# Performance work log

Hardware: AMD Instinct MI355X
Metric: run time of the kernel (lower is better)

Reference implementation:

```python
import jax, jax.numpy as jnp
import numpy as np

N_NODES = 100000
N_EDGES = 800000

def setup_inputs() -> dict:
    key = jax.random.key(0)
    ks = jax.random.split(key, 8)
    x = jax.random.normal(ks[0], (N_NODES, 500), dtype=jnp.float32)
    edge_index = jax.random.randint(ks[1], (2, N_EDGES), 0, N_NODES, dtype=jnp.int64)
    s = lambda k, shape, fan_in: jax.random.normal(k, shape, jnp.float32) / np.sqrt(fan_in)
    return {
        "x": x,
        "edge_index": edge_index,
        "W1_l": s(ks[2], (500, 20), 500),
        "W1_r": s(ks[3], (500, 20), 500),
        "b1": jnp.zeros((20,), jnp.float32),
        "W2_l": s(ks[4], (20, 3), 20),
        "W2_r": s(ks[5], (20, 3), 20),
        "b2": jnp.zeros((3,), jnp.float32),
    }

def _sage_conv(x, src, dst, W_l, W_r, b, deg_inv):
    # mean-aggregate neighbor features (x_j = x[src]) at dst, PyG default 'mean'
    agg = jax.ops.segment_sum(x[src], dst, num_segments=x.shape[0])  # [N, F]
    agg = agg * deg_inv[:, None]
    return agg @ W_l + b + x @ W_r

def reference(x, edge_index, W1_l, W1_r, b1, W2_l, W2_r, b2):
    src, dst = edge_index[0], edge_index[1]
    deg = jax.ops.segment_sum(jnp.ones_like(dst, dtype=x.dtype), dst, num_segments=x.shape[0])
    deg_inv = 1.0 / jnp.maximum(deg, 1.0)
    h = _sage_conv(x, src, dst, W1_l, W1_r, b1, deg_inv)
    h = jax.nn.relu(h)
    # F.dropout(p=0.5, training=self.training): identity in eval mode
    out = _sage_conv(h, src, dst, W2_l, W2_r, b2, deg_inv)
    return out
```

## Files before the change

kernel.cpp:

```cpp
#include <hip/hip_runtime.h>

#define F_IN  500
#define F_HID 20
#define F_OUT 3
#define KT    16
#define NT    3

typedef __attribute__((ext_vector_type(8))) short short8;
typedef __attribute__((ext_vector_type(4))) float v4f;

__device__ __forceinline__ unsigned f2bf(float f) {
    unsigned u = __float_as_uint(f);
    u = u + 0x7fffu + ((u >> 16) & 1u);
    return u >> 16;
}
__device__ __forceinline__ float bf2f(unsigned h) {
    return __uint_as_float(h << 16);
}

__global__ void k_degree(const int* __restrict__ dst, int* __restrict__ deg, int E) {
    int i = blockIdx.x * blockDim.x + threadIdx.x;
    if (i < E) atomicAdd(&deg[dst[i]], 1);
}

__global__ void k_scan_blk(const int* __restrict__ deg, int* __restrict__ rowstart,
                           int* __restrict__ blocksums, int N) {
    __shared__ int lds[256];
    int tid = threadIdx.x;
    int base = blockIdx.x * 1024 + tid * 4;
    int4 v = make_int4(0, 0, 0, 0);
    if (base + 3 < N) {
        v = *(const int4*)(deg + base);
    } else {
        if (base + 0 < N) v.x = deg[base + 0];
        if (base + 1 < N) v.y = deg[base + 1];
        if (base + 2 < N) v.z = deg[base + 2];
        if (base + 3 < N) v.w = deg[base + 3];
    }
    int tsum = v.x + v.y + v.z + v.w;
    lds[tid] = tsum;
    __syncthreads();
    for (int off = 1; off < 256; off <<= 1) {
        int t = (tid >= off) ? lds[tid - off] : 0;
        __syncthreads();
        lds[tid] += t;
        __syncthreads();
    }
    int excl = lds[tid] - tsum;
    if (tid == 255) blocksums[blockIdx.x] = lds[255];
    int r = excl;
    if (base + 0 < N) rowstart[base + 0] = r; r += v.x;
    if (base + 1 < N) rowstart[base + 1] = r; r += v.y;
    if (base + 2 < N) rowstart[base + 2] = r; r += v.z;
    if (base + 3 < N) rowstart[base + 3] = r;
}

__global__ void k_scan_sums(int* __restrict__ blocksums, int NB) {
    __shared__ int lds[256];
    int tid = threadIdx.x;
    int v = (tid < NB) ? blocksums[tid] : 0;
    lds[tid] = v;
    __syncthreads();
    for (int off = 1; off < 256; off <<= 1) {
        int t = (tid >= off) ? lds[tid - off] : 0;
        __syncthreads();
        lds[tid] += t;
        __syncthreads();
    }
    if (tid < NB) blocksums[tid] = lds[tid] - v;
}

__global__ void k_scan_add(int* __restrict__ rowstart, const int* __restrict__ blocksums, int N) {
    int i = blockIdx.x * blockDim.x + threadIdx.x;
    if (i < N) rowstart[i] += blocksums[i >> 10];
}

__global__ void k_fill(const int* __restrict__ src, const int* __restrict__ dst,
                       int* __restrict__ rowstart, int* __restrict__ csr, int E) {
    int e = blockIdx.x * blockDim.x + threadIdx.x;
    if (e >= E) return;
    int pos = atomicAdd(&rowstart[dst[e]], 1);
    csr[pos] = src[e];
}

__global__ void k_prepB(const float* __restrict__ Wl, const float* __restrict__ Wr,
                        unsigned short* __restrict__ Bhi, unsigned short* __restrict__ Blo) {
    int i = blockIdx.x * blockDim.x + threadIdx.x;
    if (i >= KT * NT * 64) return;
    int lane = i & 63;
    int ntk  = i >> 6;
    int nt   = ntk % NT;
    int kt   = ntk / NT;
    int n     = nt * 16 + (lane & 15);
    int kbase = kt * 32 + (lane >> 4) * 8;
#pragma unroll
    for (int j = 0; j < 8; ++j) {
        int k = kbase + j;
        float w = 0.f;
        if (k < F_IN && n < 2 * F_HID)
            w = (n < F_HID) ? Wl[k * F_HID + n] : Wr[k * F_HID + (n - F_HID)];
        unsigned h = f2bf(w);
        Bhi[(size_t)i * 8 + j] = (unsigned short)h;
        Blo[(size_t)i * 8 + j] = (unsigned short)f2bf(w - bf2f(h));
    }
}

__global__ __launch_bounds__(256) void k_gemm1(const float* __restrict__ x,
        const unsigned short* __restrict__ Bhi, const unsigned short* __restrict__ Blo,
        float* __restrict__ y, int N) {
    __shared__ unsigned short xhi[64 * 32];
    __shared__ unsigned short xlo[64 * 32];
    const int tid  = threadIdx.x;
    const int lane = tid & 63;
    const int wv   = tid >> 6;
    const int row0 = blockIdx.x * 64;

    v4f acc[NT];
#pragma unroll
    for (int nt = 0; nt < NT; ++nt) { acc[nt][0]=0.f; acc[nt][1]=0.f; acc[nt][2]=0.f; acc[nt][3]=0.f; }

    const int srow = tid >> 3;
    const int skc  = (tid & 7) * 4;
    const int arow = wv * 16 + (lane & 15);
    const int ak   = (lane >> 4) * 8;

    for (int kt = 0; kt < KT; ++kt) {
#pragma unroll
        for (int hh = 0; hh < 2; ++hh) {
            int rl   = srow + hh * 32;
            int grow = row0 + rl;
            int gk   = kt * 32 + skc;
            float4 v = make_float4(0.f, 0.f, 0.f, 0.f);
            if (grow < N && gk + 3 < F_IN)
                v = *(const float4*)(x + (size_t)grow * F_IN + gk);
            unsigned h0 = f2bf(v.x), h1 = f2bf(v.y), h2 = f2bf(v.z), h3 = f2bf(v.w);
            unsigned l0 = f2bf(v.x - bf2f(h0));
            unsigned l1 = f2bf(v.y - bf2f(h1));
            unsigned l2 = f2bf(v.z - bf2f(h2));
            unsigned l3 = f2bf(v.w - bf2f(h3));
            *(uint2*)&xhi[rl * 32 + skc] = make_uint2(h0 | (h1 << 16), h2 | (h3 << 16));
            *(uint2*)&xlo[rl * 32 + skc] = make_uint2(l0 | (l1 << 16), l2 | (l3 << 16));
        }
        __syncthreads();
        short8 Ah = *(const short8*)&xhi[arow * 32 + ak];
        short8 Al = *(const short8*)&xlo[arow * 32 + ak];
#pragma unroll
        for (int nt = 0; nt < NT; ++nt) {
            size_t fo = (((size_t)kt * NT + nt) * 64 + lane) * 8;
            short8 Bh = *(const short8*)(Bhi + fo);
            short8 Bl = *(const short8*)(Blo + fo);
            acc[nt] = __builtin_amdgcn_mfma_f32_16x16x32_bf16(Ah, Bh, acc[nt], 0, 0, 0);
            acc[nt] = __builtin_amdgcn_mfma_f32_16x16x32_bf16(Ah, Bl, acc[nt], 0, 0, 0);
            acc[nt] = __builtin_amdgcn_mfma_f32_16x16x32_bf16(Al, Bh, acc[nt], 0, 0, 0);
        }
        __syncthreads();
    }
    int rloc = wv * 16 + (lane >> 4) * 4;
#pragma unroll
    for (int nt = 0; nt < NT; ++nt) {
        int col = nt * 16 + (lane & 15);
        if (col < 2 * F_HID) {
#pragma unroll
            for (int rg = 0; rg < 4; ++rg) {
                int grow = row0 + rloc + rg;
                if (grow < N) y[(size_t)grow * 40 + col] = acc[nt][rg];
            }
        }
    }
}

__global__ void k_agg1(const int* __restrict__ rowend, const int* __restrict__ deg,
                       const int* __restrict__ csr, const float* __restrict__ y,
                       float* __restrict__ agg1, int N) {
    int i = blockIdx.x * blockDim.x + threadIdx.x;
    if (i >= N * 5) return;
    int n = i / 5;
    int cg = i - n * 5;
    int d = deg[n];
    int beg = rowend[n] - d;
    float4 acc = make_float4(0.f, 0.f, 0.f, 0.f);
    for (int j = 0; j < d; ++j) {
        int s = csr[beg + j];
        float4 v = *(const float4*)(y + (size_t)s * 40 + cg * 4);
        acc.x += v.x; acc.y += v.y; acc.z += v.z; acc.w += v.w;
    }
    *(float4*)(agg1 + (size_t)n * F_HID + cg * 4) = acc;
}

__global__ void k_layer1(const int* __restrict__ deg,
                         const float* __restrict__ agg1,
                         const float* __restrict__ y,
                         const float* __restrict__ b1,
                         const float* __restrict__ W2l,
                         const float* __restrict__ W2r,
                         float* __restrict__ zl, float* __restrict__ zr, int N) {
    int n = blockIdx.x * blockDim.x + threadIdx.x;
    if (n >= N) return;
    float di = 1.0f / fmaxf((float)deg[n], 1.0f);
    float h[F_HID];
    const float4* pa = (const float4*)(agg1 + (size_t)n * F_HID);
    const float4* pr = (const float4*)(y + (size_t)n * 40 + F_HID);
#pragma unroll
    for (int q = 0; q < F_HID / 4; ++q) {
        float4 a = pa[q];
        float4 r = pr[q];
        h[4*q+0] = fmaxf(a.x * di + b1[4*q+0] + r.x, 0.f);
        h[4*q+1] = fmaxf(a.y * di + b1[4*q+1] + r.y, 0.f);
        h[4*q+2] = fmaxf(a.z * di + b1[4*q+2] + r.z, 0.f);
        h[4*q+3] = fmaxf(a.w * di + b1[4*q+3] + r.w, 0.f);
    }
    float zlo[F_OUT] = {0.f, 0.f, 0.f};
    float zro[F_OUT] = {0.f, 0.f, 0.f};
#pragma unroll
    for (int c = 0; c < F_HID; ++c) {
#pragma unroll
        for (int o = 0; o < F_OUT; ++o) {
            zlo[o] += h[c] * W2l[c * F_OUT + o];
            zro[o] += h[c] * W2r[c * F_OUT + o];
        }
    }
#pragma unroll
    for (int o = 0; o < F_OUT; ++o) {
        zl[(size_t)n * F_OUT + o] = zlo[o];
        zr[(size_t)n * F_OUT + o] = zro[o];
    }
}

__global__ void k_agg2_final(const int* __restrict__ rowend, const int* __restrict__ deg,
                             const int* __restrict__ csr, const float* __restrict__ zl,
                             const float* __restrict__ zr, const float* __restrict__ b2,
                             float* __restrict__ out, int N) {
    int n = blockIdx.x * blockDim.x + threadIdx.x;
    if (n >= N) return;
    int d = deg[n];
    int beg = rowend[n] - d;
    float a0 = 0.f, a1 = 0.f, a2 = 0.f;
    for (int j = 0; j < d; ++j) {
        int s = csr[beg + j];
        const float* z = zl + (size_t)s * F_OUT;
        a0 += z[0]; a1 += z[1]; a2 += z[2];
    }
    float di = 1.0f / fmaxf((float)d, 1.0f);
    out[(size_t)n * F_OUT + 0] = a0 * di + b2[0] + zr[(size_t)n * F_OUT + 0];
    out[(size_t)n * F_OUT + 1] = a1 * di + b2[1] + zr[(size_t)n * F_OUT + 1];
    out[(size_t)n * F_OUT + 2] = a2 * di + b2[2] + zr[(size_t)n * F_OUT + 2];
}

extern "C" void kernel_launch(void* const* d_in, const int* in_sizes, int n_in,
                              void* d_out, int out_size, void* d_ws, size_t ws_size,
                              hipStream_t stream) {
    const float* x   = (const float*)d_in[0];
    const int*   ei  = (const int*)d_in[1];
    const float* W1l = (const float*)d_in[2];
    const float* W1r = (const float*)d_in[3];
    const float* b1  = (const float*)d_in[4];
    const float* W2l = (const float*)d_in[5];
    const float* W2r = (const float*)d_in[6];
    const float* b2  = (const float*)d_in[7];
    float* out = (float*)d_out;

    const int N = in_sizes[0] / F_IN;
    const int E = in_sizes[1] / 2;
    const int* src = ei;
    const int* dst = ei + E;

    int*   wsi      = (int*)d_ws;
    int*   deg      = wsi;
    int*   rowstart = deg + N;
    int*   blocksums= rowstart + N;
    int*   csr      = blocksums + 256;
    float* y        = (float*)(csr + E);
    float* agg1     = y + (size_t)N * 40;
    float* zl       = agg1 + (size_t)N * F_HID;
    float* zr       = zl + (size_t)N * F_OUT;
    unsigned short* Bhi = (unsigned short*)(zr + (size_t)N * F_OUT);
    unsigned short* Blo = Bhi + (size_t)KT * NT * 64 * 8;

    hipMemsetAsync(deg, 0, (size_t)N * sizeof(int), stream);

    const int B = 256;
    const int NB = (N + 1023) / 1024;
    k_prepB     <<<(KT * NT * 64 + B - 1) / B, B, 0, stream>>>(W1l, W1r, Bhi, Blo);
    k_degree    <<<(E + B - 1) / B, B, 0, stream>>>(dst, deg, E);
    k_scan_blk  <<<NB, 256, 0, stream>>>(deg, rowstart, blocksums, N);
    k_scan_sums <<<1, 256, 0, stream>>>(blocksums, NB);
    k_scan_add  <<<(N + B - 1) / B, B, 0, stream>>>(rowstart, blocksums, N);
    k_fill      <<<(E + B - 1) / B, B, 0, stream>>>(src, dst, rowstart, csr, E);
    k_gemm1     <<<(N + 63) / 64, 256, 0, stream>>>(x, Bhi, Blo, y, N);
    k_agg1      <<<(N * 5 + B - 1) / B, B, 0, stream>>>(rowstart, deg, csr, y, agg1, N);
    k_layer1    <<<(N + B - 1) / B, B, 0, stream>>>(deg, agg1, y, b1, W2l, W2r, zl, zr, N);
    k_agg2_final<<<(N + B - 1) / B, B, 0, stream>>>(rowstart, deg, csr, zl, zr, b2, out, N);
}
```

Baseline: 436.4 us.

## Restructure GNN pipeline: fused prep, LDS-free GEMM, fused aggregation and layer1

```diff
diff --git a/kernel.cpp b/kernel.cpp
--- a/kernel.cpp
+++ b/kernel.cpp
@@ -18,12 +18,57 @@
     return __uint_as_float(h << 16);
 }
 
-__global__ void k_degree(const int* __restrict__ dst, int* __restrict__ deg, int E) {
-    int i = blockIdx.x * blockDim.x + threadIdx.x;
-    if (i < E) atomicAdd(&deg[dst[i]], 1);
-}
-
-__global__ void k_scan_blk(const int* __restrict__ deg, int* __restrict__ rowstart,
+__device__ __forceinline__ void cvt8(const float4 p, const float4 q, short8& hi, short8& lo) {
+    float vf[8] = {p.x, p.y, p.z, p.w, q.x, q.y, q.z, q.w};
+    union { unsigned u[4]; short8 s; } H, L;
+#pragma unroll
+    for (int t = 0; t < 4; ++t) {
+        unsigned u0 = __float_as_uint(vf[2*t]);
+        unsigned u1 = __float_as_uint(vf[2*t+1]);
+        unsigned r0 = u0 + 0x7fffu + ((u0 >> 16) & 1u);
+        unsigned r1 = u1 + 0x7fffu + ((u1 >> 16) & 1u);
+        float f0 = __uint_as_float(r0 & 0xffff0000u);
+        float f1 = __uint_as_float(r1 & 0xffff0000u);
+        float d0 = vf[2*t]   - f0;
+        float d1 = vf[2*t+1] - f1;
+        unsigned s0 = __float_as_uint(d0); s0 = s0 + 0x7fffu + ((s0 >> 16) & 1u);
+        unsigned s1 = __float_as_uint(d1); s1 = s1 + 0x7fffu + ((s1 >> 16) & 1u);
+        H.u[t] = (r0 >> 16) | (r1 & 0xffff0000u);
+        L.u[t] = (s0 >> 16) | (s1 & 0xffff0000u);
+    }
+    hi = H.s; lo = L.s;
+}
+
+__global__ void k_prep(const float* __restrict__ W1l, const float* __restrict__ W1r,
+                       unsigned short* __restrict__ Bhi, unsigned short* __restrict__ Blo,
+                       const int* __restrict__ dst, int* __restrict__ deg, int E) {
+    int b = blockIdx.x;
+    int tid = threadIdx.x;
+    if (b < (KT * NT * 64) / 256) {
+        int i = b * 256 + tid;
+        int lane = i & 63;
+        int ntk  = i >> 6;
+        int nt   = ntk % NT;
+        int kt   = ntk / NT;
+        int n     = nt * 16 + (lane & 15);
+        int kbase = kt * 32 + (lane >> 4) * 8;
+#pragma unroll
+        for (int j = 0; j < 8; ++j) {
+            int k = kbase + j;
+            float w = 0.f;
+            if (k < F_IN && n < 2 * F_HID)
+                w = (n < F_HID) ? W1l[k * F_HID + n] : W1r[k * F_HID + (n - F_HID)];
+            unsigned h = f2bf(w);
+            Bhi[(size_t)i * 8 + j] = (unsigned short)h;
+            Blo[(size_t)i * 8 + j] = (unsigned short)f2bf(w - bf2f(h));
+        }
+    } else {
+        int e = (b - (KT * NT * 64) / 256) * 256 + tid;
+        if (e < E) atomicAdd(&deg[dst[e]], 1);
+    }
+}
+
+__global__ void k_scan_blk(const int* __restrict__ deg, int* __restrict__ rowloc,
                            int* __restrict__ blocksums, int N) {
     __shared__ int lds[256];
     int tid = threadIdx.x;
@@ -49,10 +94,10 @@
     int excl = lds[tid] - tsum;
     if (tid == 255) blocksums[blockIdx.x] = lds[255];
     int r = excl;
-    if (base + 0 < N) rowstart[base + 0] = r; r += v.x;
-    if (base + 1 < N) rowstart[base + 1] = r; r += v.y;
-    if (base + 2 < N) rowstart[base + 2] = r; r += v.z;
-    if (base + 3 < N) rowstart[base + 3] = r;
+    if (base + 0 < N) rowloc[base + 0] = r; r += v.x;
+    if (base + 1 < N) rowloc[base + 1] = r; r += v.y;
+    if (base + 2 < N) rowloc[base + 2] = r; r += v.z;
+    if (base + 3 < N) rowloc[base + 3] = r;
 }
 
 __global__ void k_scan_sums(int* __restrict__ blocksums, int NB) {
@@ -70,180 +115,158 @@
     if (tid < NB) blocksums[tid] = lds[tid] - v;
 }
 
-__global__ void k_scan_add(int* __restrict__ rowstart, const int* __restrict__ blocksums, int N) {
-    int i = blockIdx.x * blockDim.x + threadIdx.x;
-    if (i < N) rowstart[i] += blocksums[i >> 10];
-}
-
 __global__ void k_fill(const int* __restrict__ src, const int* __restrict__ dst,
-                       int* __restrict__ rowstart, int* __restrict__ csr, int E) {
+                       int* __restrict__ rowloc, const int* __restrict__ bs,
+                       int* __restrict__ csr, int E) {
     int e = blockIdx.x * blockDim.x + threadIdx.x;
     if (e >= E) return;
-    int pos = atomicAdd(&rowstart[dst[e]], 1);
+    int dn = dst[e];
+    int pos = atomicAdd(&rowloc[dn], 1) + bs[dn >> 10];
     csr[pos] = src[e];
-}
-
-__global__ void k_prepB(const float* __restrict__ Wl, const float* __restrict__ Wr,
-                        unsigned short* __restrict__ Bhi, unsigned short* __restrict__ Blo) {
-    int i = blockIdx.x * blockDim.x + threadIdx.x;
-    if (i >= KT * NT * 64) return;
-    int lane = i & 63;
-    int ntk  = i >> 6;
-    int nt   = ntk % NT;
-    int kt   = ntk / NT;
-    int n     = nt * 16 + (lane & 15);
-    int kbase = kt * 32 + (lane >> 4) * 8;
-#pragma unroll
-    for (int j = 0; j < 8; ++j) {
-        int k = kbase + j;
-        float w = 0.f;
-        if (k < F_IN && n < 2 * F_HID)
-            w = (n < F_HID) ? Wl[k * F_HID + n] : Wr[k * F_HID + (n - F_HID)];
-        unsigned h = f2bf(w);
-        Bhi[(size_t)i * 8 + j] = (unsigned short)h;
-        Blo[(size_t)i * 8 + j] = (unsigned short)f2bf(w - bf2f(h));
-    }
 }
 
 __global__ __launch_bounds__(256) void k_gemm1(const float* __restrict__ x,
         const unsigned short* __restrict__ Bhi, const unsigned short* __restrict__ Blo,
-        float* __restrict__ y, int N) {
-    __shared__ unsigned short xhi[64 * 32];
-    __shared__ unsigned short xlo[64 * 32];
-    const int tid  = threadIdx.x;
-    const int lane = tid & 63;
-    const int wv   = tid >> 6;
-    const int row0 = blockIdx.x * 64;
-
-    v4f acc[NT];
-#pragma unroll
-    for (int nt = 0; nt < NT; ++nt) { acc[nt][0]=0.f; acc[nt][1]=0.f; acc[nt][2]=0.f; acc[nt][3]=0.f; }
-
-    const int srow = tid >> 3;
-    const int skc  = (tid & 7) * 4;
-    const int arow = wv * 16 + (lane & 15);
-    const int ak   = (lane >> 4) * 8;
-
+        float* __restrict__ yl, float* __restrict__ yr, int N) {
+    const int lane = threadIdx.x & 63;
+    const int wv   = threadIdx.x >> 6;
+    const int fr   = lane & 15;
+    const int kq   = lane >> 4;
+    const int rowA = blockIdx.x * 128 + wv * 32;
+
+    const int r0 = min(rowA + fr,      N - 1);
+    const int r1 = min(rowA + 16 + fr, N - 1);
+    const float* __restrict__ xp0 = x + (size_t)r0 * F_IN;
+    const float* __restrict__ xp1 = x + (size_t)r1 * F_IN;
+
+    v4f acc[2][NT];
+#pragma unroll
+    for (int h = 0; h < 2; ++h)
+#pragma unroll
+        for (int nt = 0; nt < NT; ++nt)
+            acc[h][nt] = (v4f){0.f, 0.f, 0.f, 0.f};
+
+#pragma unroll 2
     for (int kt = 0; kt < KT; ++kt) {
-#pragma unroll
-        for (int hh = 0; hh < 2; ++hh) {
-            int rl   = srow + hh * 32;
-            int grow = row0 + rl;
-            int gk   = kt * 32 + skc;
-            float4 v = make_float4(0.f, 0.f, 0.f, 0.f);
-            if (grow < N && gk + 3 < F_IN)
-                v = *(const float4*)(x + (size_t)grow * F_IN + gk);
-            unsigned h0 = f2bf(v.x), h1 = f2bf(v.y), h2 = f2bf(v.z), h3 = f2bf(v.w);
-            unsigned l0 = f2bf(v.x - bf2f(h0));
-            unsigned l1 = f2bf(v.y - bf2f(h1));
-            unsigned l2 = f2bf(v.z - bf2f(h2));
-            unsigned l3 = f2bf(v.w - bf2f(h3));
-            *(uint2*)&xhi[rl * 32 + skc] = make_uint2(h0 | (h1 << 16), h2 | (h3 << 16));
-            *(uint2*)&xlo[rl * 32 + skc] = make_uint2(l0 | (l1 << 16), l2 | (l3 << 16));
-        }
-        __syncthreads();
-        short8 Ah = *(const short8*)&xhi[arow * 32 + ak];
-        short8 Al = *(const short8*)&xlo[arow * 32 + ak];
+        const int kb = kt * 32 + kq * 8;
+        const int ka = (kb     <= 496) ? kb     : 496;
+        const int kc = (kb + 4 <= 496) ? kb + 4 : 496;
+        float4 a0 = *(const float4*)(xp0 + ka);
+        float4 a1 = *(const float4*)(xp0 + kc);
+        float4 c0 = *(const float4*)(xp1 + ka);
+        float4 c1 = *(const float4*)(xp1 + kc);
+        short8 Ah0, Al0, Ah1, Al1;
+        cvt8(a0, a1, Ah0, Al0);
+        cvt8(c0, c1, Ah1, Al1);
 #pragma unroll
         for (int nt = 0; nt < NT; ++nt) {
             size_t fo = (((size_t)kt * NT + nt) * 64 + lane) * 8;
             short8 Bh = *(const short8*)(Bhi + fo);
             short8 Bl = *(const short8*)(Blo + fo);
-            acc[nt] = __builtin_amdgcn_mfma_f32_16x16x32_bf16(Ah, Bh, acc[nt], 0, 0, 0);
-            acc[nt] = __builtin_amdgcn_mfma_f32_16x16x32_bf16(Ah, Bl, acc[nt], 0, 0, 0);
-            acc[nt] = __builtin_amdgcn_mfma_f32_16x16x32_bf16(Al, Bh, acc[nt], 0, 0, 0);
+            acc[0][nt] = __builtin_amdgcn_mfma_f32_16x16x32_bf16(Ah0, Bh, acc[0][nt], 0, 0, 0);
+            acc[0][nt] = __builtin_amdgcn_mfma_f32_16x16x32_bf16(Ah0, Bl, acc[0][nt], 0, 0, 0);
+            acc[0][nt] = __builtin_amdgcn_mfma_f32_16x16x32_bf16(Al0, Bh, acc[0][nt], 0, 0, 0);
+            acc[1][nt] = __builtin_amdgcn_mfma_f32_16x16x32_bf16(Ah1, Bh, acc[1][nt], 0, 0, 0);
+            acc[1][nt] = __builtin_amdgcn_mfma_f32_16x16x32_bf16(Ah1, Bl, acc[1][nt], 0, 0, 0);
+            acc[1][nt] = __builtin_amdgcn_mfma_f32_16x16x32_bf16(Al1, Bh, acc[1][nt], 0, 0, 0);
         }
-        __syncthreads();
-    }
-    int rloc = wv * 16 + (lane >> 4) * 4;
-#pragma unroll
-    for (int nt = 0; nt < NT; ++nt) {
-        int col = nt * 16 + (lane & 15);
-        if (col < 2 * F_HID) {
-#pragma unroll
-            for (int rg = 0; rg < 4; ++rg) {
-                int grow = row0 + rloc + rg;
-                if (grow < N) y[(size_t)grow * 40 + col] = acc[nt][rg];
+    }
+#pragma unroll
+    for (int h = 0; h < 2; ++h) {
+        int rbase = rowA + h * 16 + kq * 4;
+#pragma unroll
+        for (int nt = 0; nt < NT; ++nt) {
+            int col = nt * 16 + fr;
+            if (col < 2 * F_HID) {
+#pragma unroll
+                for (int rg = 0; rg < 4; ++rg) {
+                    int grow = rbase + rg;
+                    if (grow < N) {
+                        if (col < F_HID) yl[(size_t)grow * 32 + col] = acc[h][nt][rg];
+                        else             yr[(size_t)grow * F_HID + (col - F_HID)] = acc[h][nt][rg];
+                    }
+                }
             }
         }
     }
 }
 
-__global__ void k_agg1(const int* __restrict__ rowend, const int* __restrict__ deg,
-                       const int* __restrict__ csr, const float* __restrict__ y,
-                       float* __restrict__ agg1, int N) {
-    int i = blockIdx.x * blockDim.x + threadIdx.x;
-    if (i >= N * 5) return;
-    int n = i / 5;
-    int cg = i - n * 5;
-    int d = deg[n];
-    int beg = rowend[n] - d;
-    float4 acc = make_float4(0.f, 0.f, 0.f, 0.f);
-    for (int j = 0; j < d; ++j) {
-        int s = csr[beg + j];
-        float4 v = *(const float4*)(y + (size_t)s * 40 + cg * 4);
-        acc.x += v.x; acc.y += v.y; acc.z += v.z; acc.w += v.w;
-    }
-    *(float4*)(agg1 + (size_t)n * F_HID + cg * 4) = acc;
-}
-
-__global__ void k_layer1(const int* __restrict__ deg,
-                         const float* __restrict__ agg1,
-                         const float* __restrict__ y,
-                         const float* __restrict__ b1,
-                         const float* __restrict__ W2l,
-                         const float* __restrict__ W2r,
-                         float* __restrict__ zl, float* __restrict__ zr, int N) {
+__global__ __launch_bounds__(256) void k_agg_l1(
+        const int* __restrict__ rowloc, const int* __restrict__ bs,
+        const int* __restrict__ deg, const int* __restrict__ csr,
+        const float* __restrict__ yl, const float* __restrict__ yr,
+        const float* __restrict__ b1, const float* __restrict__ W2l,
+        const float* __restrict__ W2r,
+        float* __restrict__ zl4, float* __restrict__ zr, int N) {
+    int t = blockIdx.x * blockDim.x + threadIdx.x;
+    int n = t >> 3;
+    int g = t & 7;
+    if (n >= N) return;
+    int d   = deg[n];
+    int end = rowloc[n] + bs[n >> 10];
+    int beg = end - d;
+    float4 a = make_float4(0.f, 0.f, 0.f, 0.f);
+    if (g < 5) {
+        for (int j = 0; j < d; ++j) {
+            int s = csr[beg + j];
+            float4 v = *(const float4*)(yl + (size_t)s * 32 + g * 4);
+            a.x += v.x; a.y += v.y; a.z += v.z; a.w += v.w;
+        }
+    }
+    float di = 1.0f / fmaxf((float)d, 1.0f);
+    float pl0 = 0.f, pl1 = 0.f, pl2 = 0.f, pr0 = 0.f, pr1 = 0.f, pr2 = 0.f;
+    if (g < 5) {
+        float4 bb = *(const float4*)(b1 + g * 4);
+        float4 rr = *(const float4*)(yr + (size_t)n * F_HID + g * 4);
+        float h0 = fmaxf(a.x * di + bb.x + rr.x, 0.f);
+        float h1 = fmaxf(a.y * di + bb.y + rr.y, 0.f);
+        float h2 = fmaxf(a.z * di + bb.z + rr.z, 0.f);
+        float h3 = fmaxf(a.w * di + bb.w + rr.w, 0.f);
+        const float* wl = W2l + g * 4 * F_OUT;
+        const float* wr = W2r + g * 4 * F_OUT;
+        pl0 = h0 * wl[0] + h1 * wl[3] + h2 * wl[6] + h3 * wl[9];
+        pl1 = h0 * wl[1] + h1 * wl[4] + h2 * wl[7] + h3 * wl[10];
+        pl2 = h0 * wl[2] + h1 * wl[5] + h2 * wl[8] + h3 * wl[11];
+        pr0 = h0 * wr[0] + h1 * wr[3] + h2 * wr[6] + h3 * wr[9];
+        pr1 = h0 * wr[1] + h1 * wr[4] + h2 * wr[7] + h3 * wr[10];
+        pr2 = h0 * wr[2] + h1 * wr[5] + h2 * wr[8] + h3 * wr[11];
+    }
+#pragma unroll
+    for (int m = 4; m >= 1; m >>= 1) {
+        pl0 += __shfl_xor(pl0, m);
+        pl1 += __shfl_xor(pl1, m);
+        pl2 += __shfl_xor(pl2, m);
+        pr0 += __shfl_xor(pr0, m);
+        pr1 += __shfl_xor(pr1, m);
+        pr2 += __shfl_xor(pr2, m);
+    }
+    if (g == 0) {
+        *(float4*)(zl4 + (size_t)n * 4) = make_float4(pl0, pl1, pl2, 0.f);
+        zr[(size_t)n * 3 + 0] = pr0;
+        zr[(size_t)n * 3 + 1] = pr1;
+        zr[(size_t)n * 3 + 2] = pr2;
+    }
+}
+
+__global__ void k_agg2_final(const int* __restrict__ rowloc, const int* __restrict__ bs,
+                             const int* __restrict__ deg, const int* __restrict__ csr,
+                             const float* __restrict__ zl4, const float* __restrict__ zr,
+                             const float* __restrict__ b2, float* __restrict__ out, int N) {
     int n = blockIdx.x * blockDim.x + threadIdx.x;
     if (n >= N) return;
-    float di = 1.0f / fmaxf((float)deg[n], 1.0f);
-    float h[F_HID];
-    const float4* pa = (const float4*)(agg1 + (size_t)n * F_HID);
-    const float4* pr = (const float4*)(y + (size_t)n * 40 + F_HID);
-#pragma unroll
-    for (int q = 0; q < F_HID / 4; ++q) {
-        float4 a = pa[q];
-        float4 r = pr[q];
-        h[4*q+0] = fmaxf(a.x * di + b1[4*q+0] + r.x, 0.f);
-        h[4*q+1] = fmaxf(a.y * di + b1[4*q+1] + r.y, 0.f);
-        h[4*q+2] = fmaxf(a.z * di + b1[4*q+2] + r.z, 0.f);
-        h[4*q+3] = fmaxf(a.w * di + b1[4*q+3] + r.w, 0.f);
-    }
-    float zlo[F_OUT] = {0.f, 0.f, 0.f};
-    float zro[F_OUT] = {0.f, 0.f, 0.f};
-#pragma unroll
-    for (int c = 0; c < F_HID; ++c) {
-#pragma unroll
-        for (int o = 0; o < F_OUT; ++o) {
-            zlo[o] += h[c] * W2l[c * F_OUT + o];
-            zro[o] += h[c] * W2r[c * F_OUT + o];
-        }
-    }
-#pragma unroll
-    for (int o = 0; o < F_OUT; ++o) {
-        zl[(size_t)n * F_OUT + o] = zlo[o];
-        zr[(size_t)n * F_OUT + o] = zro[o];
-    }
-}
-
-__global__ void k_agg2_final(const int* __restrict__ rowend, const int* __restrict__ deg,
-                             const int* __restrict__ csr, const float* __restrict__ zl,
-                             const float* __restrict__ zr, const float* __restrict__ b2,
-                             float* __restrict__ out, int N) {
-    int n = blockIdx.x * blockDim.x + threadIdx.x;
-    if (n >= N) return;
-    int d = deg[n];
-    int beg = rowend[n] - d;
+    int d   = deg[n];
+    int end = rowloc[n] + bs[n >> 10];
+    int beg = end - d;
     float a0 = 0.f, a1 = 0.f, a2 = 0.f;
     for (int j = 0; j < d; ++j) {
         int s = csr[beg + j];
-        const float* z = zl + (size_t)s * F_OUT;
-        a0 += z[0]; a1 += z[1]; a2 += z[2];
+        float4 z = *(const float4*)(zl4 + (size_t)s * 4);
+        a0 += z.x; a1 += z.y; a2 += z.z;
     }
     float di = 1.0f / fmaxf((float)d, 1.0f);
-    out[(size_t)n * F_OUT + 0] = a0 * di + b2[0] + zr[(size_t)n * F_OUT + 0];
-    out[(size_t)n * F_OUT + 1] = a1 * di + b2[1] + zr[(size_t)n * F_OUT + 1];
-    out[(size_t)n * F_OUT + 2] = a2 * di + b2[2] + zr[(size_t)n * F_OUT + 2];
+    out[(size_t)n * F_OUT + 0] = a0 * di + b2[0] + zr[(size_t)n * 3 + 0];
+    out[(size_t)n * F_OUT + 1] = a1 * di + b2[1] + zr[(size_t)n * 3 + 1];
+    out[(size_t)n * F_OUT + 2] = a2 * di + b2[2] + zr[(size_t)n * 3 + 2];
 }
 
 extern "C" void kernel_launch(void* const* d_in, const int* in_sizes, int n_in,
@@ -264,15 +287,15 @@
     const int* src = ei;
     const int* dst = ei + E;
 
-    int*   wsi      = (int*)d_ws;
-    int*   deg      = wsi;
-    int*   rowstart = deg + N;
-    int*   blocksums= rowstart + N;
-    int*   csr      = blocksums + 256;
-    float* y        = (float*)(csr + E);
-    float* agg1     = y + (size_t)N * 40;
-    float* zl       = agg1 + (size_t)N * F_HID;
-    float* zr       = zl + (size_t)N * F_OUT;
+    int*   wsi    = (int*)d_ws;
+    int*   deg    = wsi;
+    int*   rowloc = deg + N;
+    int*   bs     = rowloc + N;
+    int*   csr    = bs + 256;
+    float* yl     = (float*)(csr + E);
+    float* yr     = yl + (size_t)N * 32;
+    float* zl4    = yr + (size_t)N * F_HID;
+    float* zr     = zl4 + (size_t)N * 4;
     unsigned short* Bhi = (unsigned short*)(zr + (size_t)N * F_OUT);
     unsigned short* Blo = Bhi + (size_t)KT * NT * 64 * 8;
 
@@ -280,14 +303,11 @@
 
     const int B = 256;
     const int NB = (N + 1023) / 1024;
-    k_prepB     <<<(KT * NT * 64 + B - 1) / B, B, 0, stream>>>(W1l, W1r, Bhi, Blo);
-    k_degree    <<<(E + B - 1) / B, B, 0, stream>>>(dst, deg, E);
-    k_scan_blk  <<<NB, 256, 0, stream>>>(deg, rowstart, blocksums, N);
-    k_scan_sums <<<1, 256, 0, stream>>>(blocksums, NB);
-    k_scan_add  <<<(N + B - 1) / B, B, 0, stream>>>(rowstart, blocksums, N);
-    k_fill      <<<(E + B - 1) / B, B, 0, stream>>>(src, dst, rowstart, csr, E);
-    k_gemm1     <<<(N + 63) / 64, 256, 0, stream>>>(x, Bhi, Blo, y, N);
-    k_agg1      <<<(N * 5 + B - 1) / B, B, 0, stream>>>(rowstart, deg, csr, y, agg1, N);
-    k_layer1    <<<(N + B - 1) / B, B, 0, stream>>>(deg, agg1, y, b1, W2l, W2r, zl, zr, N);
-    k_agg2_final<<<(N + B - 1) / B, B, 0, stream>>>(rowstart, deg, csr, zl, zr, b2, out, N);
-}
+    k_prep      <<<(KT * NT * 64) / B + (E + B - 1) / B, B, 0, stream>>>(W1l, W1r, Bhi, Blo, dst, deg, E);
+    k_scan_blk  <<<NB, 256, 0, stream>>>(deg, rowloc, bs, N);
+    k_scan_sums <<<1, 256, 0, stream>>>(bs, NB);
+    k_fill      <<<(E + B - 1) / B, B, 0, stream>>>(src, dst, rowloc, bs, csr, E);
+    k_gemm1     <<<(N + 127) / 128, 256, 0, stream>>>(x, Bhi, Blo, yl, yr, N);
+    k_agg_l1    <<<(N * 8 + B - 1) / B, B, 0, stream>>>(rowloc, bs, deg, csr, yl, yr, b1, W2l, W2r, zl4, zr, N);
+    k_agg2_final<<<(N + B - 1) / B, B, 0, stream>>>(rowloc, bs, deg, csr, zl4, zr, b2, out, N);
+}
```

Result: slower. 447.6 us (+2.6%).
